# Optimization experiments

Measured on AMD Instinct MI355X. Metric: run time of the kernel, lower is better.

The kernel has to match this reference:

```python
import jax, jax.numpy as jnp
import numpy as np
import math

D_MODEL, N_LEVELS, N_HEADS, N_POINTS = 256, 4, 8, 4
D_HEAD = D_MODEL // N_HEADS
SPATIAL = np.array([[128, 128], [64, 64], [32, 32], [16, 16]], dtype=np.int32)  # (H_l, W_l)
LEN_IN = int((SPATIAL[:, 0] * SPATIAL[:, 1]).sum())  # 21760
N_BATCH, LEN_Q = 8, 1000


def _offset_bias():
    # torch _reset_parameters grid_init
    thetas = np.arange(N_HEADS, dtype=np.float32) * (2.0 * math.pi / N_HEADS)
    grid = np.stack([np.cos(thetas), np.sin(thetas)], -1)
    grid = grid / np.abs(grid).max(-1, keepdims=True)
    grid = np.tile(grid.reshape(N_HEADS, 1, 1, 2), (1, N_LEVELS, N_POINTS, 1))
    for i in range(N_POINTS):
        grid[:, :, i, :] *= i + 1
    return jnp.asarray(grid.reshape(-1), dtype=jnp.float32)


def setup_inputs() -> dict:
    key = jax.random.key(0)
    ks = jax.random.split(key, 8)
    s = 1.0 / math.sqrt(D_MODEL)
    return {
        "query": jax.random.normal(ks[0], (N_BATCH, LEN_Q, D_MODEL), jnp.float32),
        "reference_points": jax.random.uniform(ks[1], (N_BATCH, LEN_Q, N_LEVELS, 2), jnp.float32),
        "input_flatten": jax.random.normal(ks[2], (N_BATCH, LEN_IN, D_MODEL), jnp.float32),
        "input_spatial_shapes": jnp.asarray(SPATIAL),
        "input_level_start_index": jnp.asarray(np.concatenate([[0], np.cumsum(SPATIAL[:, 0] * SPATIAL[:, 1])[:-1]]).astype(np.int32)),
        # params (W stored as (in, out); y = x @ W + b)
        "W_off": jax.random.normal(ks[3], (D_MODEL, N_HEADS * N_LEVELS * N_POINTS * 2), jnp.float32) * 0.01,
        "b_off": _offset_bias(),
        "W_attn": jax.random.normal(ks[4], (D_MODEL, N_HEADS * N_LEVELS * N_POINTS), jnp.float32) * 0.02,
        "b_attn": jnp.zeros((N_HEADS * N_LEVELS * N_POINTS,), jnp.float32),
        "W_val": jax.random.normal(ks[5], (D_MODEL, D_MODEL), jnp.float32) * s,
        "b_val": jnp.zeros((D_MODEL,), jnp.float32),
        "W_out": jax.random.normal(ks[6], (D_MODEL, D_MODEL), jnp.float32) * s,
        "b_out": jnp.zeros((D_MODEL,), jnp.float32),
    }


def _bilinear_sample(v, x, y, H, W):
    # v: (N, nH, H*W, dH); x, y: (N, nH, Lq, nP) in pixel coords (grid_sample align_corners=False, zeros padding)
    Nb, nH, Lq, nP = x.shape
    x0 = jnp.floor(x); y0 = jnp.floor(y)
    wx1 = x - x0; wy1 = y - y0
    x0i = x0.astype(jnp.int32); y0i = y0.astype(jnp.int32)
    out = jnp.zeros((Nb, nH, Lq, nP, v.shape[-1]), v.dtype)
    for dy, wy in ((0, 1.0 - wy1), (1, wy1)):
        for dx, wx in ((0, 1.0 - wx1), (1, wx1)):
            ix = x0i + dx; iy = y0i + dy
            valid = (ix >= 0) & (ix < W) & (iy >= 0) & (iy < H)
            idx = (jnp.clip(iy, 0, H - 1) * W + jnp.clip(ix, 0, W - 1)).reshape(Nb, nH, Lq * nP, 1)
            g = jnp.take_along_axis(v, idx, axis=2).reshape(Nb, nH, Lq, nP, -1)
            out = out + g * (wy * wx * valid.astype(v.dtype))[..., None]
    return out


def reference(query, reference_points, input_flatten, input_spatial_shapes, input_level_start_index,
              W_off, b_off, W_attn, b_attn, W_val, b_val, W_out, b_out):
    shapes = np.asarray(input_spatial_shapes)          # static metadata
    starts = np.asarray(input_level_start_index)
    Nb, Lq, _ = query.shape

    value = input_flatten @ W_val + b_val              # (N, Lin, C)
    value = value.reshape(Nb, -1, N_HEADS, D_HEAD).transpose(0, 2, 1, 3)  # (N, nH, Lin, dH)

    offsets = (query @ W_off + b_off).reshape(Nb, Lq, N_HEADS, N_LEVELS, N_POINTS, 2)
    attn = jax.nn.softmax((query @ W_attn + b_attn).reshape(Nb, Lq, N_HEADS, N_LEVELS * N_POINTS), axis=-1)
    attn = attn.reshape(Nb, Lq, N_HEADS, N_LEVELS, N_POINTS)

    # normalizer is (W_l, H_l) per level; locations in [0,1]
    normalizer = jnp.asarray(np.stack([shapes[:, 1], shapes[:, 0]], -1), jnp.float32)
    loc = reference_points[:, :, None, :, None, :] + offsets / normalizer[None, None, None, :, None, :]

    out = jnp.zeros((Nb, N_HEADS, Lq, D_HEAD), value.dtype)
    for l in range(N_LEVELS):
        H, W = int(shapes[l, 0]), int(shapes[l, 1])
        s = int(starts[l])
        v_l = value[:, :, s:s + H * W]                             # (N, nH, HW, dH)
        loc_l = loc[:, :, :, l].transpose(0, 2, 1, 3, 4)           # (N, nH, Lq, nP, 2)
        x = loc_l[..., 0] * W - 0.5
        y = loc_l[..., 1] * H - 0.5
        sampled = _bilinear_sample(v_l, x, y, H, W)                # (N, nH, Lq, nP, dH)
        a_l = attn[:, :, :, l].transpose(0, 2, 1, 3)               # (N, nH, Lq, nP)
        out = out + jnp.einsum('nhqpd,nhqp->nhqd', sampled, a_l)

    out = out.transpose(0, 2, 1, 3).reshape(Nb, Lq, D_MODEL)
    return out @ W_out + b_out
```

## Files before the change

kernel.cpp:

```cpp
#include <hip/hip_runtime.h>
#include <hip/hip_bf16.h>

#define D_MODEL 256
#define N_HEADS 8
#define D_HEAD 32
#define N_LEVELS 4
#define N_POINTS 4
#define LEN_IN 21760
#define N_BATCH 8
#define LEN_Q 1000

typedef __attribute__((ext_vector_type(8))) short short8;
typedef __attribute__((ext_vector_type(4))) float f32x4;
typedef __attribute__((ext_vector_type(4))) unsigned int u32x4;

typedef const __attribute__((address_space(1))) void* gp1;
typedef __attribute__((address_space(3))) void* lp3;

__device__ __forceinline__ unsigned short f2bf(float f) {
    unsigned int u = __float_as_uint(f);
    u += 0x7FFFu + ((u >> 16) & 1u);
    return (unsigned short)(u >> 16);
}
__device__ __forceinline__ float bf2f(unsigned short s) {
    return __uint_as_float(((unsigned int)s) << 16);
}

__global__ __launch_bounds__(256) void prep_kernel(
    const float* __restrict__ Wv, const float* __restrict__ Wo,
    const float* __restrict__ Wa, const float* __restrict__ Wu,
    const float* __restrict__ boff, const float* __restrict__ battn,
    unsigned short* __restrict__ WtVp, unsigned short* __restrict__ WtC,
    unsigned short* __restrict__ WtO, float* __restrict__ bcat)
{
    int idx = blockIdx.x * 256 + threadIdx.x;
    if (idx < 65536) {
        int j = idx & 7, lane = (idx >> 3) & 63, nf = (idx >> 9) & 15, ks = idx >> 13;
        int col = nf * 16 + (lane & 15);
        int k = ks * 32 + (lane >> 4) * 8 + j;
        WtVp[idx] = f2bf(Wv[k * 256 + col]);
    } else if (idx < 65536 + 98304) {
        int j = idx - 65536;
        int n = j >> 8, k = j & 255;
        float s = (n < 256) ? Wo[k * 256 + n] : Wa[k * 128 + (n - 256)];
        WtC[j] = f2bf(s);
    } else if (idx < 65536 + 98304 + 65536) {
        int j = idx - (65536 + 98304);
        int n = j >> 8, k = j & 255;
        WtO[j] = f2bf(Wu[k * 256 + n]);
    } else if (idx < 65536 + 98304 + 65536 + 384) {
        int j = idx - (65536 + 98304 + 65536);
        bcat[j] = (j < 256) ? boff[j] : battn[j - 256];
    }
}

__global__ __launch_bounds__(256) void gemm_value(
    const float* __restrict__ A,
    const unsigned short* __restrict__ Bp,
    const float* __restrict__ bias,
    unsigned short* __restrict__ C)
{
    __shared__ float lds[3][2048];

    const int tid = threadIdx.x;
    const int wave = tid >> 6, lane = tid & 63;
    const int lhi = lane >> 4, llo = lane & 15;
    const int mBase = blockIdx.x * 64;

    const int soff = tid * 16;
    const int r0 = soff >> 7, cb0 = soff & 127;
    const size_t g0 = (size_t)r0 * 1024 + (size_t)(cb0 ^ ((r0 & 7) << 4));
    const size_t g1 = g0 + (size_t)32 * 1024;
    const char* Ab = (const char*)(A + (size_t)mBase * 256);
    const int dsto = soff >> 2;

#define STAGE(t) { \
        float* dst0 = &lds[(t) % 3][dsto]; \
        const size_t off_ = (size_t)(t) * 128; \
        __builtin_amdgcn_global_load_lds((gp1)(const void*)(Ab + off_ + g0), \
                                         (lp3)dst0, 16, 0, 0); \
        __builtin_amdgcn_global_load_lds((gp1)(const void*)(Ab + off_ + g1), \
                                         (lp3)(dst0 + 1024), 16, 0, 0); }

    f32x4 acc[4][4];
#pragma unroll
    for (int mf = 0; mf < 4; ++mf)
#pragma unroll
        for (int n = 0; n < 4; ++n)
            acc[mf][n] = (f32x4){0.f, 0.f, 0.f, 0.f};

    short8 bcur[4], bnxt[4];

#pragma unroll
    for (int n = 0; n < 4; ++n)
        bcur[n] = *reinterpret_cast<const short8*>(
            Bp + ((size_t)(0 * 16 + wave * 4 + n) * 64 + lane) * 8);
    STAGE(0);
    STAGE(1);

#pragma unroll
    for (int kt = 0; kt < 8; ++kt) {
        if (kt < 7) {
#pragma unroll
            for (int n = 0; n < 4; ++n)
                bnxt[n] = *reinterpret_cast<const short8*>(
                    Bp + ((size_t)((kt + 1) * 16 + wave * 4 + n) * 64 + lane) * 8);
        }
        if (kt < 6) STAGE(kt + 2);

        __builtin_amdgcn_sched_barrier(0);
        if (kt < 6)      asm volatile("s_waitcnt vmcnt(8)" ::: "memory");
        else if (kt == 6) asm volatile("s_waitcnt vmcnt(6)" ::: "memory");
        else              asm volatile("s_waitcnt vmcnt(0)" ::: "memory");
        __builtin_amdgcn_sched_barrier(0);
        __builtin_amdgcn_s_barrier();
        __builtin_amdgcn_sched_barrier(0);

        short8 af[4];
#pragma unroll
        for (int mf = 0; mf < 4; ++mf) {
            const int row = mf * 16 + llo;
            const int sz = (llo & 7) << 4;
            const char* base = (const char*)&lds[kt % 3][0] + row * 128;
            f32x4 flo = *reinterpret_cast<const f32x4*>(base + ((lhi * 32) ^ sz));
            f32x4 fhi = *reinterpret_cast<const f32x4*>(base + ((lhi * 32 + 16) ^ sz));
            short8 t;
            t[0] = (short)f2bf(flo[0]); t[1] = (short)f2bf(flo[1]);
            t[2] = (short)f2bf(flo[2]); t[3] = (short)f2bf(flo[3]);
            t[4] = (short)f2bf(fhi[0]); t[5] = (short)f2bf(fhi[1]);
            t[6] = (short)f2bf(fhi[2]); t[7] = (short)f2bf(fhi[3]);
            af[mf] = t;
        }

#pragma unroll
        for (int mf = 0; mf < 4; ++mf)
#pragma unroll
            for (int n = 0; n < 4; ++n)
                acc[mf][n] = __builtin_amdgcn_mfma_f32_16x16x32_bf16(
                    af[mf], bcur[n], acc[mf][n], 0, 0, 0);

        if (kt < 7) {
#pragma unroll
            for (int n = 0; n < 4; ++n) bcur[n] = bnxt[n];
        }

        __builtin_amdgcn_sched_barrier(0);
        __builtin_amdgcn_s_barrier();
        __builtin_amdgcn_sched_barrier(0);
    }
#undef STAGE

#pragma unroll
    for (int mf = 0; mf < 4; ++mf) {
        const int row0 = mBase + mf * 16 + lhi * 4;
#pragma unroll
        for (int n = 0; n < 4; ++n) {
            const int col = wave * 64 + n * 16 + llo;
            const float bb = bias[col];
#pragma unroll
            for (int r = 0; r < 4; ++r)
                C[(size_t)(row0 + r) * 256 + col] = f2bf(acc[mf][n][r] + bb);
        }
    }
}

template<int NF, bool ABF16, bool OBF16>
__global__ __launch_bounds__(256) void gemm_k256(
    const void* __restrict__ Av, const unsigned short* __restrict__ Wt,
    const float* __restrict__ bias, void* __restrict__ Cv)
{
    const int wave = threadIdx.x >> 6;
    const int lane = threadIdx.x & 63;
    const int lhi = lane >> 4, llo = lane & 15;
    const int mBase = blockIdx.x * 16;
    const int colBase = wave * (NF * 16);
    const int N = NF * 64;

    f32x4 acc[NF];
#pragma unroll
    for (int n = 0; n < NF; ++n)
        acc[n] = (f32x4){0.f, 0.f, 0.f, 0.f};

#pragma unroll
    for (int ks = 0; ks < 8; ++ks) {
        const int kk = ks * 32 + lhi * 8;
        short8 a;
        if (ABF16) {
            a = *reinterpret_cast<const short8*>(
                (const unsigned short*)Av + (size_t)(mBase + llo) * 256 + kk);
        } else {
            const float* ap = (const float*)Av + (size_t)(mBase + llo) * 256 + kk;
            f32x4 f0 = *reinterpret_cast<const f32x4*>(ap);
            f32x4 f1 = *reinterpret_cast<const f32x4*>(ap + 4);
            short8 t;
            t[0] = (short)f2bf(f0[0]); t[1] = (short)f2bf(f0[1]);
            t[2] = (short)f2bf(f0[2]); t[3] = (short)f2bf(f0[3]);
            t[4] = (short)f2bf(f1[0]); t[5] = (short)f2bf(f1[1]);
            t[6] = (short)f2bf(f1[2]); t[7] = (short)f2bf(f1[3]);
            a = t;
        }
        short8 b[NF];
#pragma unroll
        for (int n = 0; n < NF; ++n) {
            const unsigned short* bp =
                Wt + (size_t)(colBase + n * 16 + llo) * 256 + kk;
            b[n] = *reinterpret_cast<const short8*>(bp);
        }
#pragma unroll
        for (int n = 0; n < NF; ++n)
            acc[n] = __builtin_amdgcn_mfma_f32_16x16x32_bf16(
                a, b[n], acc[n], 0, 0, 0);
    }

    const int row0 = mBase + lhi * 4;
#pragma unroll
    for (int n = 0; n < NF; ++n) {
        const int col = colBase + n * 16 + llo;
        const float bb = bias[col];
#pragma unroll
        for (int r = 0; r < 4; ++r) {
            float v = acc[n][r] + bb;
            size_t idx = (size_t)(row0 + r) * N + col;
            if (OBF16) ((unsigned short*)Cv)[idx] = f2bf(v);
            else       ((float*)Cv)[idx] = v;
        }
    }
}

__global__ __launch_bounds__(512) void ms_sample_kernel(
    const unsigned short* __restrict__ value,
    const float* __restrict__ proj,
    const float* __restrict__ refp,
    unsigned short* __restrict__ out_h)
{
    const int bid = blockIdx.x;
    const int b = bid & 7;
    const int q = bid >> 3;
    const int bq = b * LEN_Q + q;

    const int h = threadIdx.x >> 6;
    const int lane = threadIdx.x & 63;
    const int task = lane >> 2;
    const int l = task >> 2;
    const int qd = lane & 3;

    const float* prow = proj + (size_t)bq * 384;

    const int Wl = 128 >> l;
    const int st = (65536 - (65536 >> (l << 1))) / 3;

    const float2 dxy = *reinterpret_cast<const float2*>(prow + h * 32 + 2 * task);
    const float2 rxy = *reinterpret_cast<const float2*>(refp + ((size_t)bq * 4 + l) * 2);

    const float Wlf = (float)Wl;
    const float x = rxy.x * Wlf + dxy.x - 0.5f;
    const float y = rxy.y * Wlf + dxy.y - 0.5f;
    const float x0f = floorf(x), y0f = floorf(y);
    const int x0 = (int)x0f, y0 = (int)y0f;
    const float wx1 = x - x0f, wy1 = y - y0f;
    const float wx0 = 1.f - wx1, wy0 = 1.f - wy1;

    const int x0c = min(max(x0, 0), Wl - 1);
    const int x1c = min(max(x0 + 1, 0), Wl - 1);
    const int y0c = min(max(y0, 0), Wl - 1);
    const int y1c = min(max(y0 + 1, 0), Wl - 1);
    const float fx0 = (x0 >= 0 && x0 < Wl) ? 1.f : 0.f;
    const float fx1 = (x0 + 1 >= 0 && x0 + 1 < Wl) ? 1.f : 0.f;
    const float fy0 = (y0 >= 0 && y0 < Wl) ? 1.f : 0.f;
    const float fy1 = (y0 + 1 >= 0 && y0 + 1 < Wl) ? 1.f : 0.f;

    const int rr0 = st + y0c * Wl, rr1 = st + y1c * Wl;
    const int r00 = rr0 + x0c, r01 = rr0 + x1c;
    const int r10 = rr1 + x0c, r11 = rr1 + x1c;

    const char* vb = (const char*)value + (size_t)b * LEN_IN * 512
                   + h * 64 + qd * 16;
    u32x4 v0 = *reinterpret_cast<const u32x4*>(vb + (size_t)r00 * 512);
    u32x4 v1 = *reinterpret_cast<const u32x4*>(vb + (size_t)r01 * 512);
    u32x4 v2 = *reinterpret_cast<const u32x4*>(vb + (size_t)r10 * 512);
    u32x4 v3 = *reinterpret_cast<const u32x4*>(vb + (size_t)r11 * 512);

    float lg = prow[256 + h * 16 + (lane & 15)];
    float mx = lg;
    mx = fmaxf(mx, __shfl_xor(mx, 1, 16));
    mx = fmaxf(mx, __shfl_xor(mx, 2, 16));
    mx = fmaxf(mx, __shfl_xor(mx, 4, 16));
    mx = fmaxf(mx, __shfl_xor(mx, 8, 16));
    float e = __expf(lg - mx);
    float den = e;
    den += __shfl_xor(den, 1, 16);
    den += __shfl_xor(den, 2, 16);
    den += __shfl_xor(den, 4, 16);
    den += __shfl_xor(den, 8, 16);
    const float wsm = e / den;
    const float ws = __shfl(wsm, task, 16);

    float wgt[4];
    wgt[0] = ws * wy0 * wx0 * fy0 * fx0;
    wgt[1] = ws * wy0 * wx1 * fy0 * fx1;
    wgt[2] = ws * wy1 * wx0 * fy1 * fx0;
    wgt[3] = ws * wy1 * wx1 * fy1 * fx1;

    float acc[8];
#pragma unroll
    for (int j = 0; j < 8; ++j) acc[j] = 0.f;
#pragma unroll
    for (int n = 0; n < 4; ++n) {
        const u32x4 v = (n == 0) ? v0 : (n == 1) ? v1 : (n == 2) ? v2 : v3;
        const float wn = wgt[n];
#pragma unroll
        for (int j = 0; j < 4; ++j) {
            const unsigned int u = v[j];
            acc[2 * j]     += wn * bf2f((unsigned short)(u & 0xFFFFu));
            acc[2 * j + 1] += wn * bf2f((unsigned short)(u >> 16));
        }
    }

#pragma unroll
    for (int j = 0; j < 8; ++j) {
        acc[j] += __shfl_xor(acc[j], 4, 64);
        acc[j] += __shfl_xor(acc[j], 8, 64);
        acc[j] += __shfl_xor(acc[j], 16, 64);
        acc[j] += __shfl_xor(acc[j], 32, 64);
    }

    if (task == 0) {
        u32x4 o;
#pragma unroll
        for (int j = 0; j < 4; ++j)
            o[j] = (unsigned int)f2bf(acc[2 * j]) |
                   ((unsigned int)f2bf(acc[2 * j + 1]) << 16);
        *reinterpret_cast<u32x4*>(
            out_h + (size_t)bq * 256 + h * 32 + qd * 8) = o;
    }
}

extern "C" void kernel_launch(void* const* d_in, const int* in_sizes, int n_in,
                              void* d_out, int out_size, void* d_ws, size_t ws_size,
                              hipStream_t stream)
{
    const float* query  = (const float*)d_in[0];
    const float* refp   = (const float*)d_in[1];
    const float* inpf   = (const float*)d_in[2];
    const float* W_off  = (const float*)d_in[5];
    const float* b_off  = (const float*)d_in[6];
    const float* W_attn = (const float*)d_in[7];
    const float* b_attn = (const float*)d_in[8];
    const float* W_val  = (const float*)d_in[9];
    const float* b_val  = (const float*)d_in[10];
    const float* W_out  = (const float*)d_in[11];
    const float* b_out  = (const float*)d_in[12];

    char* ws = (char*)d_ws;
    unsigned short* value = (unsigned short*)(ws);
    float*          proj  = (float*)(ws + 89128960);
    unsigned short* out_h = (unsigned short*)(ws + 89128960 + 12288000);
    unsigned short* WtVp  = (unsigned short*)(ws + 109608960);
    unsigned short* WtC   = (unsigned short*)(ws + 109740032);
    unsigned short* WtO   = (unsigned short*)(ws + 109936640);
    float*          bcat  = (float*)(ws + 110067712);

    prep_kernel<<<898, 256, 0, stream>>>(W_val, W_off, W_attn, W_out,
                                         b_off, b_attn, WtVp, WtC, WtO, bcat);

    gemm_value<<<(N_BATCH * LEN_IN) / 64, 256, 0, stream>>>(
        inpf, WtVp, b_val, value);

    gemm_k256<6, false, false><<<(N_BATCH * LEN_Q) / 16, 256, 0, stream>>>(
        query, WtC, bcat, (void*)proj);

    ms_sample_kernel<<<N_BATCH * LEN_Q, 512, 0, stream>>>(
        value, proj, refp, out_h);

    gemm_k256<4, true, false><<<(N_BATCH * LEN_Q) / 16, 256, 0, stream>>>(
        out_h, WtO, b_out, d_out);
}
```

Baseline: 137.2 us.

## Give each wave private rows and all columns in the value GEMM

The value-projection GEMM is restructured so that each wave owns 32 rows (two 16-row tiles) and all 256 output columns. Each wave stages its own activation rows into a private double-buffered LDS slice, which removes the block-wide barriers and the three-stage shared pipeline. The grid changes to 1360 blocks. In exchange, every wave now reloads the full bf16 weight matrix from global/L2 for each 16-row tile, about four times the previous B traffic, and each lane holds more registers.

New measurement: 185.4 us. +35.2%, slower.

```diff
diff --git a/kernel.cpp b/kernel.cpp
--- a/kernel.cpp
+++ b/kernel.cpp
@@ -60,108 +60,77 @@
     const float* __restrict__ bias,
     unsigned short* __restrict__ C)
 {
-    __shared__ float lds[3][2048];
+    __shared__ float lds[4][2][512];
 
     const int tid = threadIdx.x;
-    const int wave = tid >> 6, lane = tid & 63;
+    const int wv = tid >> 6, lane = tid & 63;
     const int lhi = lane >> 4, llo = lane & 15;
-    const int mBase = blockIdx.x * 64;
-
-    const int soff = tid * 16;
-    const int r0 = soff >> 7, cb0 = soff & 127;
-    const size_t g0 = (size_t)r0 * 1024 + (size_t)(cb0 ^ ((r0 & 7) << 4));
-    const size_t g1 = g0 + (size_t)32 * 1024;
-    const char* Ab = (const char*)(A + (size_t)mBase * 256);
-    const int dsto = soff >> 2;
-
-#define STAGE(t) { \
-        float* dst0 = &lds[(t) % 3][dsto]; \
-        const size_t off_ = (size_t)(t) * 128; \
-        __builtin_amdgcn_global_load_lds((gp1)(const void*)(Ab + off_ + g0), \
-                                         (lp3)dst0, 16, 0, 0); \
-        __builtin_amdgcn_global_load_lds((gp1)(const void*)(Ab + off_ + g1), \
-                                         (lp3)(dst0 + 1024), 16, 0, 0); }
-
-    f32x4 acc[4][4];
-#pragma unroll
-    for (int mf = 0; mf < 4; ++mf)
-#pragma unroll
-        for (int n = 0; n < 4; ++n)
-            acc[mf][n] = (f32x4){0.f, 0.f, 0.f, 0.f};
-
-    short8 bcur[4], bnxt[4];
-
-#pragma unroll
-    for (int n = 0; n < 4; ++n)
-        bcur[n] = *reinterpret_cast<const short8*>(
-            Bp + ((size_t)(0 * 16 + wave * 4 + n) * 64 + lane) * 8);
-    STAGE(0);
-    STAGE(1);
-
-#pragma unroll
-    for (int kt = 0; kt < 8; ++kt) {
-        if (kt < 7) {
-#pragma unroll
-            for (int n = 0; n < 4; ++n)
-                bnxt[n] = *reinterpret_cast<const short8*>(
-                    Bp + ((size_t)((kt + 1) * 16 + wave * 4 + n) * 64 + lane) * 8);
-        }
-        if (kt < 6) STAGE(kt + 2);
-
-        __builtin_amdgcn_sched_barrier(0);
-        if (kt < 6)      asm volatile("s_waitcnt vmcnt(8)" ::: "memory");
-        else if (kt == 6) asm volatile("s_waitcnt vmcnt(6)" ::: "memory");
-        else              asm volatile("s_waitcnt vmcnt(0)" ::: "memory");
-        __builtin_amdgcn_sched_barrier(0);
-        __builtin_amdgcn_s_barrier();
-        __builtin_amdgcn_sched_barrier(0);
-
-        short8 af[4];
-#pragma unroll
-        for (int mf = 0; mf < 4; ++mf) {
-            const int row = mf * 16 + llo;
+    const size_t rowBase = ((size_t)blockIdx.x * 4 + wv) * 32;
+
+    const int sr = lane >> 3;
+    const int sco = (((lane & 7) << 4) ^ ((sr & 7) << 4));
+    const char* Ab = (const char*)(A + rowBase * 256);
+
+#define STG(bi, koff) { \
+        const char* s0_ = At + (size_t)sr * 1024 + (size_t)(koff) + sco; \
+        float* d0_ = &lds[wv][bi][lane << 2]; \
+        __builtin_amdgcn_global_load_lds((gp1)(const void*)s0_, (lp3)d0_, 16, 0, 0); \
+        __builtin_amdgcn_global_load_lds((gp1)(const void*)(s0_ + 8192), \
+                                         (lp3)(d0_ + 256), 16, 0, 0); }
+
+#pragma unroll
+    for (int t = 0; t < 2; ++t) {
+        const char* At = Ab + t * 16384;
+
+        f32x4 acc[16];
+#pragma unroll
+        for (int nf = 0; nf < 16; ++nf)
+            acc[nf] = (f32x4){0.f, 0.f, 0.f, 0.f};
+
+        STG(0, 0);
+
+#pragma unroll
+        for (int ks = 0; ks < 8; ++ks) {
+            short8 b[16];
+#pragma unroll
+            for (int nf = 0; nf < 16; ++nf)
+                b[nf] = *reinterpret_cast<const short8*>(
+                    Bp + ((size_t)(ks * 16 + nf) * 64 + lane) * 8);
+
+            if (ks < 7) STG((ks + 1) & 1, (ks + 1) * 128);
+
+            __builtin_amdgcn_sched_barrier(0);
+            if (ks < 7) asm volatile("s_waitcnt vmcnt(18)" ::: "memory");
+            else        asm volatile("s_waitcnt vmcnt(16)" ::: "memory");
+            __builtin_amdgcn_sched_barrier(0);
+
+            const char* base = (const char*)&lds[wv][ks & 1][0] + llo * 128;
             const int sz = (llo & 7) << 4;
-            const char* base = (const char*)&lds[kt % 3][0] + row * 128;
             f32x4 flo = *reinterpret_cast<const f32x4*>(base + ((lhi * 32) ^ sz));
             f32x4 fhi = *reinterpret_cast<const f32x4*>(base + ((lhi * 32 + 16) ^ sz));
-            short8 t;
-            t[0] = (short)f2bf(flo[0]); t[1] = (short)f2bf(flo[1]);
-            t[2] = (short)f2bf(flo[2]); t[3] = (short)f2bf(flo[3]);
-            t[4] = (short)f2bf(fhi[0]); t[5] = (short)f2bf(fhi[1]);
-            t[6] = (short)f2bf(fhi[2]); t[7] = (short)f2bf(fhi[3]);
-            af[mf] = t;
-        }
-
-#pragma unroll
-        for (int mf = 0; mf < 4; ++mf)
-#pragma unroll
-            for (int n = 0; n < 4; ++n)
-                acc[mf][n] = __builtin_amdgcn_mfma_f32_16x16x32_bf16(
-                    af[mf], bcur[n], acc[mf][n], 0, 0, 0);
-
-        if (kt < 7) {
-#pragma unroll
-            for (int n = 0; n < 4; ++n) bcur[n] = bnxt[n];
-        }
-
-        __builtin_amdgcn_sched_barrier(0);
-        __builtin_amdgcn_s_barrier();
-        __builtin_amdgcn_sched_barrier(0);
-    }
-#undef STAGE
-
-#pragma unroll
-    for (int mf = 0; mf < 4; ++mf) {
-        const int row0 = mBase + mf * 16 + lhi * 4;
-#pragma unroll
-        for (int n = 0; n < 4; ++n) {
-            const int col = wave * 64 + n * 16 + llo;
+            short8 af;
+            af[0] = (short)f2bf(flo[0]); af[1] = (short)f2bf(flo[1]);
+            af[2] = (short)f2bf(flo[2]); af[3] = (short)f2bf(flo[3]);
+            af[4] = (short)f2bf(fhi[0]); af[5] = (short)f2bf(fhi[1]);
+            af[6] = (short)f2bf(fhi[2]); af[7] = (short)f2bf(fhi[3]);
+
+#pragma unroll
+            for (int nf = 0; nf < 16; ++nf)
+                acc[nf] = __builtin_amdgcn_mfma_f32_16x16x32_bf16(
+                    af, b[nf], acc[nf], 0, 0, 0);
+        }
+
+        const int row0 = (int)rowBase + t * 16 + lhi * 4;
+#pragma unroll
+        for (int nf = 0; nf < 16; ++nf) {
+            const int col = nf * 16 + llo;
             const float bb = bias[col];
 #pragma unroll
             for (int r = 0; r < 4; ++r)
-                C[(size_t)(row0 + r) * 256 + col] = f2bf(acc[mf][n][r] + bb);
-        }
-    }
+                C[(size_t)(row0 + r) * 256 + col] = f2bf(acc[nf][r] + bb);
+        }
+    }
+#undef STG
 }
 
 template<int NF, bool ABF16, bool OBF16>
@@ -363,8 +332,7 @@
     prep_kernel<<<898, 256, 0, stream>>>(W_val, W_off, W_attn, W_out,
                                          b_off, b_attn, WtVp, WtC, WtO, bcat);
 
-    gemm_value<<<(N_BATCH * LEN_IN) / 64, 256, 0, stream>>>(
-        inpf, WtVp, b_val, value);
+    gemm_value<<<1360, 256, 0, stream>>>(inpf, WtVp, b_val, value);
 
     gemm_k256<6, false, false><<<(N_BATCH * LEN_Q) / 16, 256, 0, stream>>>(
         query, WtC, bcat, (void*)proj);
```

## Restage value GEMM with 64-wide K double buffer and packed bf16 conversion

Applied to the files above, without the earlier changes.

The value projection GEMM moves from a triple-buffered 32-wide K pipeline (8 iterations) to a double-buffered 64-wide K pipeline (4 iterations) with a new XOR swizzle, so there are fewer barriers per tile. Software f32-to-bf16 rounding is replaced by the hardware v_cvt_pk_bf16_f32 instruction in both GEMMs and in the epilogue, which cuts ALU work in the A-operand conversion. The bias loads are also hoisted out of the epilogue loop. The cost is less prefetch depth and more LDS per block (32KB).

After: 128.5 us. 6.3% less time.

```diff
diff --git a/kernel.cpp b/kernel.cpp
--- a/kernel.cpp
+++ b/kernel.cpp
@@ -24,6 +24,11 @@
 }
 __device__ __forceinline__ float bf2f(unsigned short s) {
     return __uint_as_float(((unsigned int)s) << 16);
+}
+__device__ __forceinline__ unsigned int cvtpk(float lo, float hi) {
+    unsigned int r;
+    asm("v_cvt_pk_bf16_f32 %0, %1, %2" : "=v"(r) : "v"(lo), "v"(hi));
+    return r;
 }
 
 __global__ __launch_bounds__(256) void prep_kernel(
@@ -60,27 +65,24 @@
     const float* __restrict__ bias,
     unsigned short* __restrict__ C)
 {
-    __shared__ float lds[3][2048];
+    __shared__ __align__(16) float lds[2][4096];
 
     const int tid = threadIdx.x;
     const int wave = tid >> 6, lane = tid & 63;
     const int lhi = lane >> 4, llo = lane & 15;
     const int mBase = blockIdx.x * 64;
 
-    const int soff = tid * 16;
-    const int r0 = soff >> 7, cb0 = soff & 127;
-    const size_t g0 = (size_t)r0 * 1024 + (size_t)(cb0 ^ ((r0 & 7) << 4));
-    const size_t g1 = g0 + (size_t)32 * 1024;
+    const int srow = tid >> 4;
+    const int scg = (tid & 15) ^ (srow & 15);
     const char* Ab = (const char*)(A + (size_t)mBase * 256);
-    const int dsto = soff >> 2;
-
-#define STAGE(t) { \
-        float* dst0 = &lds[(t) % 3][dsto]; \
-        const size_t off_ = (size_t)(t) * 128; \
-        __builtin_amdgcn_global_load_lds((gp1)(const void*)(Ab + off_ + g0), \
-                                         (lp3)dst0, 16, 0, 0); \
-        __builtin_amdgcn_global_load_lds((gp1)(const void*)(Ab + off_ + g1), \
-                                         (lp3)(dst0 + 1024), 16, 0, 0); }
+
+#define STG(bi, kt) { \
+    const char* s_ = Ab + (size_t)(kt) * 256 + (size_t)srow * 1024 + scg * 16; \
+    char* d_ = (char*)&lds[bi][0] + tid * 16; \
+    __builtin_amdgcn_global_load_lds((gp1)(const void*)(s_),         (lp3)(d_),         16, 0, 0); \
+    __builtin_amdgcn_global_load_lds((gp1)(const void*)(s_ + 16384), (lp3)(d_ + 4096),  16, 0, 0); \
+    __builtin_amdgcn_global_load_lds((gp1)(const void*)(s_ + 32768), (lp3)(d_ + 8192),  16, 0, 0); \
+    __builtin_amdgcn_global_load_lds((gp1)(const void*)(s_ + 49152), (lp3)(d_ + 12288), 16, 0, 0); }
 
     f32x4 acc[4][4];
 #pragma unroll
@@ -89,77 +91,72 @@
         for (int n = 0; n < 4; ++n)
             acc[mf][n] = (f32x4){0.f, 0.f, 0.f, 0.f};
 
-    short8 bcur[4], bnxt[4];
-
-#pragma unroll
-    for (int n = 0; n < 4; ++n)
-        bcur[n] = *reinterpret_cast<const short8*>(
-            Bp + ((size_t)(0 * 16 + wave * 4 + n) * 64 + lane) * 8);
-    STAGE(0);
-    STAGE(1);
-
-#pragma unroll
-    for (int kt = 0; kt < 8; ++kt) {
-        if (kt < 7) {
+    STG(0, 0);
+
+#pragma unroll
+    for (int kt = 0; kt < 4; ++kt) {
+        const int cur = kt & 1;
+
+        short8 b[2][4];
+#pragma unroll
+        for (int ksi = 0; ksi < 2; ++ksi)
 #pragma unroll
             for (int n = 0; n < 4; ++n)
-                bnxt[n] = *reinterpret_cast<const short8*>(
-                    Bp + ((size_t)((kt + 1) * 16 + wave * 4 + n) * 64 + lane) * 8);
-        }
-        if (kt < 6) STAGE(kt + 2);
-
-        __builtin_amdgcn_sched_barrier(0);
-        if (kt < 6)      asm volatile("s_waitcnt vmcnt(8)" ::: "memory");
-        else if (kt == 6) asm volatile("s_waitcnt vmcnt(6)" ::: "memory");
-        else              asm volatile("s_waitcnt vmcnt(0)" ::: "memory");
+                b[ksi][n] = *reinterpret_cast<const short8*>(
+                    Bp + ((size_t)((kt * 2 + ksi) * 16 + wave * 4 + n) * 64 + lane) * 8);
+
+        if (kt < 3) STG(cur ^ 1, kt + 1);
+
+        __builtin_amdgcn_sched_barrier(0);
+        if (kt < 3) asm volatile("s_waitcnt vmcnt(12)" ::: "memory");
+        else        asm volatile("s_waitcnt vmcnt(8)" ::: "memory");
         __builtin_amdgcn_sched_barrier(0);
         __builtin_amdgcn_s_barrier();
         __builtin_amdgcn_sched_barrier(0);
 
-        short8 af[4];
 #pragma unroll
         for (int mf = 0; mf < 4; ++mf) {
             const int row = mf * 16 + llo;
-            const int sz = (llo & 7) << 4;
-            const char* base = (const char*)&lds[kt % 3][0] + row * 128;
-            f32x4 flo = *reinterpret_cast<const f32x4*>(base + ((lhi * 32) ^ sz));
-            f32x4 fhi = *reinterpret_cast<const f32x4*>(base + ((lhi * 32 + 16) ^ sz));
-            short8 t;
-            t[0] = (short)f2bf(flo[0]); t[1] = (short)f2bf(flo[1]);
-            t[2] = (short)f2bf(flo[2]); t[3] = (short)f2bf(flo[3]);
-            t[4] = (short)f2bf(fhi[0]); t[5] = (short)f2bf(fhi[1]);
-            t[6] = (short)f2bf(fhi[2]); t[7] = (short)f2bf(fhi[3]);
-            af[mf] = t;
-        }
-
-#pragma unroll
-        for (int mf = 0; mf < 4; ++mf)
-#pragma unroll
-            for (int n = 0; n < 4; ++n)
-                acc[mf][n] = __builtin_amdgcn_mfma_f32_16x16x32_bf16(
-                    af[mf], bcur[n], acc[mf][n], 0, 0, 0);
-
-        if (kt < 7) {
-#pragma unroll
-            for (int n = 0; n < 4; ++n) bcur[n] = bnxt[n];
+            const char* rbase = (const char*)&lds[cur][0] + row * 256;
+#pragma unroll
+            for (int ksi = 0; ksi < 2; ++ksi) {
+                const int cg0 = ksi * 8 + lhi * 2;
+                f32x4 flo = *reinterpret_cast<const f32x4*>(rbase + ((cg0 ^ llo) << 4));
+                f32x4 fhi = *reinterpret_cast<const f32x4*>(rbase + (((cg0 + 1) ^ llo) << 4));
+                u32x4 pk;
+                pk[0] = cvtpk(flo[0], flo[1]);
+                pk[1] = cvtpk(flo[2], flo[3]);
+                pk[2] = cvtpk(fhi[0], fhi[1]);
+                pk[3] = cvtpk(fhi[2], fhi[3]);
+                short8 af = __builtin_bit_cast(short8, pk);
+#pragma unroll
+                for (int n = 0; n < 4; ++n)
+                    acc[mf][n] = __builtin_amdgcn_mfma_f32_16x16x32_bf16(
+                        af, b[ksi][n], acc[mf][n], 0, 0, 0);
+            }
         }
 
         __builtin_amdgcn_sched_barrier(0);
         __builtin_amdgcn_s_barrier();
         __builtin_amdgcn_sched_barrier(0);
     }
-#undef STAGE
-
+#undef STG
+
+    float bb[4];
+#pragma unroll
+    for (int n = 0; n < 4; ++n) bb[n] = bias[wave * 64 + n * 16 + llo];
 #pragma unroll
     for (int mf = 0; mf < 4; ++mf) {
         const int row0 = mBase + mf * 16 + lhi * 4;
 #pragma unroll
         for (int n = 0; n < 4; ++n) {
             const int col = wave * 64 + n * 16 + llo;
-            const float bb = bias[col];
-#pragma unroll
-            for (int r = 0; r < 4; ++r)
-                C[(size_t)(row0 + r) * 256 + col] = f2bf(acc[mf][n][r] + bb);
+            unsigned int u01 = cvtpk(acc[mf][n][0] + bb[n], acc[mf][n][1] + bb[n]);
+            unsigned int u23 = cvtpk(acc[mf][n][2] + bb[n], acc[mf][n][3] + bb[n]);
+            C[(size_t)(row0 + 0) * 256 + col] = (unsigned short)(u01 & 0xFFFFu);
+            C[(size_t)(row0 + 1) * 256 + col] = (unsigned short)(u01 >> 16);
+            C[(size_t)(row0 + 2) * 256 + col] = (unsigned short)(u23 & 0xFFFFu);
+            C[(size_t)(row0 + 3) * 256 + col] = (unsigned short)(u23 >> 16);
         }
     }
 }
@@ -192,12 +189,12 @@
             const float* ap = (const float*)Av + (size_t)(mBase + llo) * 256 + kk;
             f32x4 f0 = *reinterpret_cast<const f32x4*>(ap);
             f32x4 f1 = *reinterpret_cast<const f32x4*>(ap + 4);
-            short8 t;
-            t[0] = (short)f2bf(f0[0]); t[1] = (short)f2bf(f0[1]);
-            t[2] = (short)f2bf(f0[2]); t[3] = (short)f2bf(f0[3]);
-            t[4] = (short)f2bf(f1[0]); t[5] = (short)f2bf(f1[1]);
-            t[6] = (short)f2bf(f1[2]); t[7] = (short)f2bf(f1[3]);
-            a = t;
+            u32x4 pk;
+            pk[0] = cvtpk(f0[0], f0[1]);
+            pk[1] = cvtpk(f0[2], f0[3]);
+            pk[2] = cvtpk(f1[0], f1[1]);
+            pk[3] = cvtpk(f1[2], f1[3]);
+            a = __builtin_bit_cast(short8, pk);
         }
         short8 b[NF];
 #pragma unroll
```
